# Performance work log

Measured on AMD Instinct MI355X. Metric: run time of the kernel, lower is better.

## Reference

```python
import jax, jax.numpy as jnp
import numpy as np

IN1, IN2, OUT = 256, 64, 64

def setup_inputs() -> dict:
    key = jax.random.key(0)
    k1, k2, k3, k4 = jax.random.split(key, 4)
    x1 = jax.random.normal(k1, (4, 4096, IN1), dtype=jnp.float32)
    x2 = jax.random.normal(k2, (4, 4096, IN2), dtype=jnp.float32)
    # nn.Linear(in_1, in_2*out): weight (in_2*out, in_1), bias (in_2*out,)
    W = jax.random.normal(k3, (IN2 * OUT, IN1), dtype=jnp.float32) / np.sqrt(IN1)
    bvec = jax.random.normal(k4, (IN2 * OUT,), dtype=jnp.float32) * 0.01
    return {"x1": x1, "x2": x2, "W": W, "bvec": bvec}

def reference(x1, x2, W, bvec):
    b, n, _ = x1.shape
    # per-token generated weight: (b, n, in_2, out)
    w = (jnp.einsum('bni,oi->bno', x1, W) + bvec).reshape(b, n, IN2, OUT)
    # batched vector-matrix product per token
    y = jnp.einsum('bnj,bnjo->bno', x2, w)
    return y
```

## Files before the change

### kernel.cpp

```cpp
#include <hip/hip_runtime.h>


#define FRAGS 16
#define FRAG_SHORTS 512
#define JF_SHORTS (FRAGS * FRAG_SHORTS)

typedef __bf16 bf16x8 __attribute__((ext_vector_type(8)));
typedef float  f32x16 __attribute__((ext_vector_type(16)));

static __device__ __forceinline__ unsigned short f2bf(float f) {
  union { float f; unsigned u; } v; v.f = f;
  unsigned r = v.u + 0x7FFFu + ((v.u >> 16) & 1u);
  return (unsigned short)(r >> 16);
}

static __device__ __forceinline__ void gload_lds16(const unsigned short* g,
                                                   unsigned short* l) {
  __builtin_amdgcn_global_load_lds(
      (const __attribute__((address_space(1))) void*)g,
      (__attribute__((address_space(3))) void*)l, 16, 0, 0);
}

__global__ void prep_w(const float* __restrict__ W,
                       unsigned short* __restrict__ Wf) {
  int idx = blockIdx.x * 256 + threadIdx.x;
  int r  = idx >> 4;
  int ks = idx & 15;
  int j   = r >> 6;
  int o   = r & 63;
  int oh  = o >> 5;
  int l31 = o & 31;
  size_t fb = ((size_t)(j * 2 + oh) * FRAGS + ks) * FRAG_SHORTS;

  const float4* row = (const float4*)(W + (size_t)r * 256 + ks * 16);
  float4 v0 = row[0], v1 = row[1], v2 = row[2], v3 = row[3];
  ushort4 lo0, lo1, hi0, hi1;
  lo0.x = f2bf(v0.x); lo0.y = f2bf(v0.y); lo0.z = f2bf(v0.z); lo0.w = f2bf(v0.w);
  lo1.x = f2bf(v1.x); lo1.y = f2bf(v1.y); lo1.z = f2bf(v1.z); lo1.w = f2bf(v1.w);
  hi0.x = f2bf(v2.x); hi0.y = f2bf(v2.y); hi0.z = f2bf(v2.z); hi0.w = f2bf(v2.w);
  hi1.x = f2bf(v3.x); hi1.y = f2bf(v3.y); hi1.z = f2bf(v3.z); hi1.w = f2bf(v3.w);
  *(ushort4*)&Wf[fb + l31 * 8 + 0] = lo0;
  *(ushort4*)&Wf[fb + l31 * 8 + 4] = lo1;
  *(ushort4*)&Wf[fb + 256 + l31 * 8 + 0] = hi0;
  *(ushort4*)&Wf[fb + 256 + l31 * 8 + 4] = hi1;
}

__global__ void prep_bias(const float* __restrict__ x2,
                          const float* __restrict__ bv,
                          float* __restrict__ out) {
  __shared__ float sbv[4096];
  __shared__ float sx2[256];
  int tid = threadIdx.x;
  #pragma unroll
  for (int i = 0; i < 16; ++i) sbv[i * 256 + tid] = bv[i * 256 + tid];
  long t0 = (long)blockIdx.x * 4;
  sx2[tid] = x2[t0 * 64 + tid];
  __syncthreads();
  int o = tid & 63, tl = tid >> 6;
  float acc = 0.f;
  #pragma unroll
  for (int j = 0; j < 64; ++j) acc += sx2[tl * 64 + j] * sbv[j * 64 + o];
  out[(t0 + tl) * 64 + o] = acc;
}

__global__ __launch_bounds__(256, 2)
void meta_main(const float* __restrict__ x1, const float* __restrict__ x2,
               const unsigned short* __restrict__ Wf, float* __restrict__ out) {
  __shared__ unsigned short sWf[4 * JF_SHORTS];
  __shared__ float sX2[64 * 64];

  const int tid  = threadIdx.x;
  const int lane = tid & 63;
  const int wv   = tid >> 6;
  const int th   = wv & 1;
  const int jh   = wv >> 1;
  const int l31  = lane & 31;
  const int lg   = lane >> 5;

  const int bid  = blockIdx.x;
  const int oh   = (bid >> 3) & 1;
  const int tile = (bid & 7) + ((bid >> 4) << 3);
  const long tile0 = (long)tile * 64;

  {
    unsigned short* sX1 = sWf;
    const float4* src = (const float4*)(x1 + tile0 * 256);
    #pragma unroll
    for (int it = 0; it < 16; ++it) {
      int fi4 = it * 256 + tid;
      float4 v = src[fi4];
      int token = fi4 >> 6;
      int col   = (fi4 & 63) * 4;
      ushort4 b;
      b.x = f2bf(v.x); b.y = f2bf(v.y); b.z = f2bf(v.z); b.w = f2bf(v.w);
      *(ushort4*)&sX1[token * 264 + col] = b;
    }
    const float4* s2 = (const float4*)(x2 + tile0 * 64);
    #pragma unroll
    for (int it = 0; it < 4; ++it) {
      int fi4 = it * 256 + tid;
      float4 v = s2[fi4];
      int token = fi4 >> 4;
      int j0    = (fi4 & 15) * 4;
      sX2[(j0 + 0) * 64 + token] = v.x;
      sX2[(j0 + 1) * 64 + token] = v.y;
      sX2[(j0 + 2) * 64 + token] = v.z;
      sX2[(j0 + 3) * 64 + token] = v.w;
    }
  }
  __syncthreads();

  bf16x8 bfrag[FRAGS];
  {
    const unsigned short* base = &sWf[(32 * th + l31) * 264 + lg * 8];
    #pragma unroll
    for (int ks = 0; ks < FRAGS; ++ks)
      bfrag[ks] = *(const bf16x8*)(base + ks * 16);
  }
  __syncthreads();

  const int jbase = jh * 32;
  unsigned short* ring = &sWf[jh * 2 * JF_SHORTS];
  const unsigned short* wlane =
      Wf + ((size_t)(jbase * 2 + oh)) * JF_SHORTS + lane * 8;

  if (th == 0) {
    #pragma unroll
    for (int ks = 0; ks < FRAGS; ++ks)
      gload_lds16(wlane + ks * FRAG_SHORTS, &ring[ks * FRAG_SHORTS]);
  }
  __syncthreads();

  f32x16 yacc;
  #pragma unroll
  for (int r = 0; r < 16; ++r) yacc[r] = 0.0f;

  const int tt = 32 * th + l31;

  #pragma unroll 2
  for (int jl = 0; jl < 32; ++jl) {
    const int buf = jl & 1;
    if (th == 0 && jl + 1 < 32) {
      const unsigned short* p = wlane + (size_t)(jl + 1) * 2 * JF_SHORTS;
      unsigned short* d = &ring[(buf ^ 1) * JF_SHORTS];
      #pragma unroll
      for (int ks = 0; ks < FRAGS; ++ks)
        gload_lds16(p + ks * FRAG_SHORTS, d + ks * FRAG_SHORTS);
    }
    const unsigned short* rb = &ring[buf * JF_SHORTS] + lane * 8;
    f32x16 wlo, whi;
    #pragma unroll
    for (int r = 0; r < 16; ++r) { wlo[r] = 0.0f; whi[r] = 0.0f; }
    #pragma unroll
    for (int ks = 0; ks < 8; ++ks) {
      bf16x8 wk = *(const bf16x8*)(rb + ks * FRAG_SHORTS);
      wlo = __builtin_amdgcn_mfma_f32_32x32x16_bf16(wk, bfrag[ks], wlo, 0, 0, 0);
    }
    #pragma unroll
    for (int ks = 8; ks < 16; ++ks) {
      bf16x8 wk = *(const bf16x8*)(rb + ks * FRAG_SHORTS);
      whi = __builtin_amdgcn_mfma_f32_32x32x16_bf16(wk, bfrag[ks], whi, 0, 0, 0);
    }
    float x2s = sX2[(jbase + jl) * 64 + tt];
    #pragma unroll
    for (int r = 0; r < 16; ++r) yacc[r] += x2s * (wlo[r] + whi[r]);
    __syncthreads();
  }

  float* red = (float*)sWf;
  if (jh == 1) {
    #pragma unroll
    for (int r = 0; r < 16; ++r) red[(th * 64 + lane) * 17 + r] = yacc[r];
  }
  __syncthreads();
  if (jh == 0) {
    const float* rd = &red[(th * 64 + lane) * 17];
    float* yout = out + (tile0 + tt) * 64 + oh * 32;
    #pragma unroll
    for (int r = 0; r < 16; ++r) {
      int ol = (r & 3) + 8 * (r >> 2) + 4 * lg;
      yout[ol] += yacc[r] + rd[r];
    }
  }
}

extern "C" void kernel_launch(void* const* d_in, const int* in_sizes, int n_in,
                              void* d_out, int out_size, void* d_ws, size_t ws_size,
                              hipStream_t stream) {
  const float* x1 = (const float*)d_in[0];
  const float* x2 = (const float*)d_in[1];
  const float* W  = (const float*)d_in[2];
  const float* bv = (const float*)d_in[3];
  float* y = (float*)d_out;
  unsigned short* Wf = (unsigned short*)d_ws;

  prep_w<<<256, 256, 0, stream>>>(W, Wf);
  prep_bias<<<4096, 256, 0, stream>>>(x2, bv, y);
  meta_main<<<512, 256, 0, stream>>>(x1, x2, Wf, y);
}
```

Baseline: 119.5 us.

## Double token tile per block, fold bias into MFMA, drop bias kernel

The main kernel now runs 512 threads per block on 128-token tiles. Each streamed W fragment feeds two MFMAs (tokens A and B), which halves W traffic per token, and four j-quarter waves are reduced through LDS at the end. The separate prep_bias kernel is removed. The bias term is computed as an extra bf16 MFMA from a pre-swizzled bias fragment, and the output is written directly with float4 stores instead of read-modify-write. In exchange it uses 160KB of LDS and more registers, which may limit occupancy, and the bias and x2 terms are now computed at bf16 precision.

```diff
diff --git a/kernel.cpp b/kernel.cpp
--- a/kernel.cpp
+++ b/kernel.cpp
@@ -4,6 +4,7 @@
 #define FRAGS 16
 #define FRAG_SHORTS 512
 #define JF_SHORTS (FRAGS * FRAG_SHORTS)
+#define BIAS_OFF ((size_t)(64 * 2 * FRAGS) * FRAG_SHORTS)
 
 typedef __bf16 bf16x8 __attribute__((ext_vector_type(8)));
 typedef float  f32x16 __attribute__((ext_vector_type(16)));
@@ -21,7 +22,7 @@
       (__attribute__((address_space(3))) void*)l, 16, 0, 0);
 }
 
-__global__ void prep_w(const float* __restrict__ W,
+__global__ void prep_w(const float* __restrict__ W, const float* __restrict__ bv,
                        unsigned short* __restrict__ Wf) {
   int idx = blockIdx.x * 256 + threadIdx.x;
   int r  = idx >> 4;
@@ -43,31 +44,25 @@
   *(ushort4*)&Wf[fb + l31 * 8 + 4] = lo1;
   *(ushort4*)&Wf[fb + 256 + l31 * 8 + 0] = hi0;
   *(ushort4*)&Wf[fb + 256 + l31 * 8 + 4] = hi1;
-}
-
-__global__ void prep_bias(const float* __restrict__ x2,
-                          const float* __restrict__ bv,
-                          float* __restrict__ out) {
-  __shared__ float sbv[4096];
-  __shared__ float sx2[256];
-  int tid = threadIdx.x;
-  #pragma unroll
-  for (int i = 0; i < 16; ++i) sbv[i * 256 + tid] = bv[i * 256 + tid];
-  long t0 = (long)blockIdx.x * 4;
-  sx2[tid] = x2[t0 * 64 + tid];
-  __syncthreads();
-  int o = tid & 63, tl = tid >> 6;
-  float acc = 0.f;
-  #pragma unroll
-  for (int j = 0; j < 64; ++j) acc += sx2[tl * 64 + j] * sbv[j * 64 + o];
-  out[(t0 + tl) * 64 + o] = acc;
-}
-
-__global__ __launch_bounds__(256, 2)
+
+  if (idx < 512) {
+    int f   = idx >> 6;
+    int ln  = idx & 63;
+    int ohb = f >> 2, jhb = f & 3;
+    int lb  = ln & 31, lgb = ln >> 5;
+    #pragma unroll
+    for (int e = 0; e < 8; ++e)
+      Wf[BIAS_OFF + (size_t)f * FRAG_SHORTS + ln * 8 + e] =
+          f2bf(bv[(jhb * 16 + 8 * lgb + e) * 64 + 32 * ohb + lb]);
+  }
+}
+
+__global__ __launch_bounds__(512, 2)
 void meta_main(const float* __restrict__ x1, const float* __restrict__ x2,
                const unsigned short* __restrict__ Wf, float* __restrict__ out) {
-  __shared__ unsigned short sWf[4 * JF_SHORTS];
-  __shared__ float sX2[64 * 64];
+  __shared__ __align__(16) unsigned char smem[163840];
+  unsigned short* sWf = (unsigned short*)smem;
+  float* sX2 = (float*)(smem + 131072);
 
   const int tid  = threadIdx.x;
   const int lane = tid & 63;
@@ -78,108 +73,139 @@
   const int lg   = lane >> 5;
 
   const int bid  = blockIdx.x;
-  const int oh   = (bid >> 3) & 1;
-  const int tile = (bid & 7) + ((bid >> 4) << 3);
-  const long tile0 = (long)tile * 64;
+  const int xcd  = bid & 7;
+  const int kk   = bid >> 3;
+  const int tile = xcd * 16 + (kk >> 1);
+  const int oh   = kk & 1;
+  const long tile0 = (long)tile * 128;
 
   {
-    unsigned short* sX1 = sWf;
     const float4* src = (const float4*)(x1 + tile0 * 256);
     #pragma unroll
     for (int it = 0; it < 16; ++it) {
-      int fi4 = it * 256 + tid;
+      int fi4 = it * 512 + tid;
       float4 v = src[fi4];
       int token = fi4 >> 6;
       int col   = (fi4 & 63) * 4;
       ushort4 b;
       b.x = f2bf(v.x); b.y = f2bf(v.y); b.z = f2bf(v.z); b.w = f2bf(v.w);
-      *(ushort4*)&sX1[token * 264 + col] = b;
+      *(ushort4*)&sWf[token * 264 + col] = b;
     }
     const float4* s2 = (const float4*)(x2 + tile0 * 64);
     #pragma unroll
     for (int it = 0; it < 4; ++it) {
-      int fi4 = it * 256 + tid;
+      int fi4 = it * 512 + tid;
       float4 v = s2[fi4];
       int token = fi4 >> 4;
       int j0    = (fi4 & 15) * 4;
-      sX2[(j0 + 0) * 64 + token] = v.x;
-      sX2[(j0 + 1) * 64 + token] = v.y;
-      sX2[(j0 + 2) * 64 + token] = v.z;
-      sX2[(j0 + 3) * 64 + token] = v.w;
-    }
-  }
-  __syncthreads();
-
-  bf16x8 bfrag[FRAGS];
+      sX2[(j0 + 0) * 128 + token] = v.x;
+      sX2[(j0 + 1) * 128 + token] = v.y;
+      sX2[(j0 + 2) * 128 + token] = v.z;
+      sX2[(j0 + 3) * 128 + token] = v.w;
+    }
+  }
+  __syncthreads();
+
+  const int tA = th * 64 + l31;
+  const int tB = tA + 32;
+
+  bf16x8 bfA[16], bfB[16];
+  #pragma unroll
+  for (int ks = 0; ks < 16; ++ks) {
+    bfA[ks] = *(const bf16x8*)&sWf[tA * 264 + ks * 16 + lg * 8];
+    bfB[ks] = *(const bf16x8*)&sWf[tB * 264 + ks * 16 + lg * 8];
+  }
+
+  f32x16 yA, yB;
   {
-    const unsigned short* base = &sWf[(32 * th + l31) * 264 + lg * 8];
-    #pragma unroll
-    for (int ks = 0; ks < FRAGS; ++ks)
-      bfrag[ks] = *(const bf16x8*)(base + ks * 16);
-  }
-  __syncthreads();
-
-  const int jbase = jh * 32;
-  unsigned short* ring = &sWf[jh * 2 * JF_SHORTS];
-  const unsigned short* wlane =
-      Wf + ((size_t)(jbase * 2 + oh)) * JF_SHORTS + lane * 8;
-
-  if (th == 0) {
-    #pragma unroll
-    for (int ks = 0; ks < FRAGS; ++ks)
-      gload_lds16(wlane + ks * FRAG_SHORTS, &ring[ks * FRAG_SHORTS]);
-  }
-  __syncthreads();
-
-  f32x16 yacc;
-  #pragma unroll
-  for (int r = 0; r < 16; ++r) yacc[r] = 0.0f;
-
-  const int tt = 32 * th + l31;
+    union { bf16x8 v; unsigned short u[8]; } xfA, xfB;
+    #pragma unroll
+    for (int e = 0; e < 8; ++e) {
+      int jrow = jh * 16 + 8 * lg + e;
+      xfA.u[e] = f2bf(sX2[jrow * 128 + tA]);
+      xfB.u[e] = f2bf(sX2[jrow * 128 + tB]);
+    }
+    bf16x8 biasA = *(const bf16x8*)(Wf + BIAS_OFF +
+                                    (size_t)(oh * 4 + jh) * FRAG_SHORTS + lane * 8);
+    f32x16 z;
+    #pragma unroll
+    for (int r2 = 0; r2 < 16; ++r2) z[r2] = 0.0f;
+    yA = __builtin_amdgcn_mfma_f32_32x32x16_bf16(biasA, xfA.v, z, 0, 0, 0);
+    yB = __builtin_amdgcn_mfma_f32_32x32x16_bf16(biasA, xfB.v, z, 0, 0, 0);
+  }
+  __syncthreads();
+
+  unsigned short* ring = sWf + jh * (2 * JF_SHORTS);
+  const int ks0 = th * 8;
+
+  {
+    const unsigned short* src =
+        Wf + ((size_t)((jh * 16) * 2 + oh) * FRAGS + ks0) * FRAG_SHORTS + lane * 8;
+    unsigned short* dst = ring + ks0 * FRAG_SHORTS;
+    #pragma unroll
+    for (int q = 0; q < 8; ++q)
+      gload_lds16(src + q * FRAG_SHORTS, dst + q * FRAG_SHORTS);
+  }
+  __syncthreads();
 
   #pragma unroll 2
-  for (int jl = 0; jl < 32; ++jl) {
-    const int buf = jl & 1;
-    if (th == 0 && jl + 1 < 32) {
-      const unsigned short* p = wlane + (size_t)(jl + 1) * 2 * JF_SHORTS;
-      unsigned short* d = &ring[(buf ^ 1) * JF_SHORTS];
+  for (int i = 0; i < 16; ++i) {
+    const int buf = i & 1;
+    if (i + 1 < 16) {
+      const int jn = jh * 16 + i + 1;
+      const unsigned short* src =
+          Wf + ((size_t)(jn * 2 + oh) * FRAGS + ks0) * FRAG_SHORTS + lane * 8;
+      unsigned short* dst = ring + (buf ^ 1) * JF_SHORTS + ks0 * FRAG_SHORTS;
       #pragma unroll
-      for (int ks = 0; ks < FRAGS; ++ks)
-        gload_lds16(p + ks * FRAG_SHORTS, d + ks * FRAG_SHORTS);
-    }
-    const unsigned short* rb = &ring[buf * JF_SHORTS] + lane * 8;
-    f32x16 wlo, whi;
-    #pragma unroll
-    for (int r = 0; r < 16; ++r) { wlo[r] = 0.0f; whi[r] = 0.0f; }
-    #pragma unroll
-    for (int ks = 0; ks < 8; ++ks) {
+      for (int q = 0; q < 8; ++q)
+        gload_lds16(src + q * FRAG_SHORTS, dst + q * FRAG_SHORTS);
+    }
+    const unsigned short* rb = ring + buf * JF_SHORTS + lane * 8;
+    f32x16 aA, aB;
+    #pragma unroll
+    for (int r2 = 0; r2 < 16; ++r2) { aA[r2] = 0.0f; aB[r2] = 0.0f; }
+    #pragma unroll
+    for (int ks = 0; ks < 16; ++ks) {
       bf16x8 wk = *(const bf16x8*)(rb + ks * FRAG_SHORTS);
-      wlo = __builtin_amdgcn_mfma_f32_32x32x16_bf16(wk, bfrag[ks], wlo, 0, 0, 0);
-    }
-    #pragma unroll
-    for (int ks = 8; ks < 16; ++ks) {
-      bf16x8 wk = *(const bf16x8*)(rb + ks * FRAG_SHORTS);
-      whi = __builtin_amdgcn_mfma_f32_32x32x16_bf16(wk, bfrag[ks], whi, 0, 0, 0);
-    }
-    float x2s = sX2[(jbase + jl) * 64 + tt];
-    #pragma unroll
-    for (int r = 0; r < 16; ++r) yacc[r] += x2s * (wlo[r] + whi[r]);
+      aA = __builtin_amdgcn_mfma_f32_32x32x16_bf16(wk, bfA[ks], aA, 0, 0, 0);
+      aB = __builtin_amdgcn_mfma_f32_32x32x16_bf16(wk, bfB[ks], aB, 0, 0, 0);
+    }
+    const int j = jh * 16 + i;
+    const float xA = sX2[j * 128 + tA];
+    const float xB = sX2[j * 128 + tB];
+    #pragma unroll
+    for (int r2 = 0; r2 < 16; ++r2) {
+      yA[r2] += xA * aA[r2];
+      yB[r2] += xB * aB[r2];
+    }
     __syncthreads();
   }
 
   float* red = (float*)sWf;
-  if (jh == 1) {
-    #pragma unroll
-    for (int r = 0; r < 16; ++r) red[(th * 64 + lane) * 17 + r] = yacc[r];
+  const int sA = ((th * 2 + 0) * 64 + lane) * 4 + jh;
+  const int sB = ((th * 2 + 1) * 64 + lane) * 4 + jh;
+  if (jh != 0) {
+    #pragma unroll
+    for (int r2 = 0; r2 < 16; ++r2) {
+      red[sA * 17 + r2] = yA[r2];
+      red[sB * 17 + r2] = yB[r2];
+    }
   }
   __syncthreads();
   if (jh == 0) {
-    const float* rd = &red[(th * 64 + lane) * 17];
-    float* yout = out + (tile0 + tt) * 64 + oh * 32;
-    #pragma unroll
-    for (int r = 0; r < 16; ++r) {
-      int ol = (r & 3) + 8 * (r >> 2) + 4 * lg;
-      yout[ol] += yacc[r] + rd[r];
+    #pragma unroll
+    for (int r2 = 0; r2 < 16; ++r2) {
+      yA[r2] += red[(sA + 1) * 17 + r2] + red[(sA + 2) * 17 + r2] + red[(sA + 3) * 17 + r2];
+      yB[r2] += red[(sB + 1) * 17 + r2] + red[(sB + 2) * 17 + r2] + red[(sB + 3) * 17 + r2];
+    }
+    float* yoA = out + (tile0 + tA) * 64 + oh * 32;
+    float* yoB = out + (tile0 + tB) * 64 + oh * 32;
+    #pragma unroll
+    for (int rq = 0; rq < 4; ++rq) {
+      float4 vA = make_float4(yA[4 * rq + 0], yA[4 * rq + 1], yA[4 * rq + 2], yA[4 * rq + 3]);
+      float4 vB = make_float4(yB[4 * rq + 0], yB[4 * rq + 1], yB[4 * rq + 2], yB[4 * rq + 3]);
+      *(float4*)(yoA + 8 * rq + 4 * lg) = vA;
+      *(float4*)(yoB + 8 * rq + 4 * lg) = vB;
     }
   }
 }
@@ -194,7 +220,6 @@
   float* y = (float*)d_out;
   unsigned short* Wf = (unsigned short*)d_ws;
 
-  prep_w<<<256, 256, 0, stream>>>(W, Wf);
-  prep_bias<<<4096, 256, 0, stream>>>(x2, bv, y);
-  meta_main<<<512, 256, 0, stream>>>(x1, x2, Wf, y);
-}
+  prep_w<<<256, 256, 0, stream>>>(W, bv, Wf);
+  meta_main<<<256, 512, 0, stream>>>(x1, x2, Wf, y);
+}
```

Result: faster. 105.6 us (-11.7%).
